# Kernel tuning notes

Measured on AMD Instinct MI355X. Metric: run time of the kernel, lower is better.

Reference implementation:

```python
import jax, jax.numpy as jnp
import numpy as np

N_NODES = 100000
N_EDGES = 1600000
IN_DIM = 128
HEADS = 4
CHANNELS = 32          # hidden_size // heads = 128 // 4
OUT_DIM = 32           # output_size of last GATConv
NEG_SLOPE = 0.2        # DGL GATConv default leaky_relu slope


def setup_inputs() -> dict:
    key = jax.random.key(0)
    ks = jax.random.split(key, 16)
    x = jax.random.normal(ks[0], (N_NODES, IN_DIM), dtype=jnp.float32)
    src = jax.random.randint(ks[1], (N_EDGES,), 0, N_NODES, dtype=jnp.int32)
    dst = jax.random.randint(ks[2], (N_EDGES,), 0, N_NODES, dtype=jnp.int32)

    def glorot(k, shape):
        fan = shape[0] + shape[-1]
        return jax.random.normal(k, shape, dtype=jnp.float32) * np.sqrt(2.0 / fan)

    # layer 0: in=128 -> 4 heads x 32
    W1 = glorot(ks[3], (IN_DIM, HEADS * CHANNELS))
    al1 = glorot(ks[4], (HEADS, CHANNELS))
    ar1 = glorot(ks[5], (HEADS, CHANNELS))
    W2 = glorot(ks[6], (HEADS * CHANNELS, HEADS * CHANNELS))
    al2 = glorot(ks[7], (HEADS, CHANNELS))
    ar2 = glorot(ks[8], (HEADS, CHANNELS))
    W3 = glorot(ks[9], (HEADS * CHANNELS, HEADS * OUT_DIM))
    al3 = glorot(ks[10], (HEADS, OUT_DIM))
    ar3 = glorot(ks[11], (HEADS, OUT_DIM))
    # final FC: (output_size*heads=128) -> 8
    Wfc = glorot(ks[12], (HEADS * OUT_DIM, 8))
    bfc = jnp.zeros((8,), dtype=jnp.float32)
    return {"x": x, "src": src, "dst": dst,
            "W1": W1, "al1": al1, "ar1": ar1,
            "W2": W2, "al2": al2, "ar2": ar2,
            "W3": W3, "al3": al3, "ar3": ar3,
            "Wfc": Wfc, "bfc": bfc}


def gat_layer(x, W, a_l, a_r, src, dst, activation):
    """DGL-style GATConv: fused gather / attend / segment-softmax / scatter-add."""
    n = x.shape[0]
    h, c = a_l.shape
    feat = (x @ W).reshape(n, h, c)                       # [N,H,C]
    el = jnp.einsum("nhc,hc->nh", feat, a_l)               # [N,H]
    er = jnp.einsum("nhc,hc->nh", feat, a_r)               # [N,H]
    e = jax.nn.leaky_relu(el[src] + er[dst], NEG_SLOPE)    # [E,H] per-edge logits
    # segment softmax over incoming edges of each dst node
    emax = jax.ops.segment_max(e, dst, num_segments=n)     # [N,H]
    ee = jnp.exp(e - emax[dst])                            # [E,H]
    denom = jax.ops.segment_sum(ee, dst, num_segments=n)   # [N,H]
    alpha = ee / denom[dst]                                # [E,H]
    msg = feat[src] * alpha[:, :, None]                    # [E,H,C]
    out = jax.ops.segment_sum(msg, dst, num_segments=n)    # [N,H,C]
    if activation is not None:
        out = activation(out)
    return out.reshape(n, h * c)


def reference(x, src, dst, W1, al1, ar1, W2, al2, ar2, W3, al3, ar3, Wfc, bfc):
    src = src.astype(jnp.int32)
    dst = dst.astype(jnp.int32)
    h = gat_layer(x, W1, al1, ar1, src, dst, jax.nn.relu)
    h = gat_layer(h, W2, al2, ar2, src, dst, jax.nn.relu)
    h = gat_layer(h, W3, al3, ar3, src, dst, None)         # [N, OUT_DIM*HEADS]
    h = jax.nn.relu(h)                                     # dropout p=0 -> identity
    pooled = jnp.max(h, axis=0, keepdims=True)             # graph max-pool readout [1, 128]
    logits = pooled @ Wfc + bfc                            # [1, 8]
    return jax.nn.softmax(logits, axis=-1)
```

## Files before the change

### kernel.cpp

```cpp
#include <hip/hip_runtime.h>

#define NN 100000
#define NE 1600000
#define FD 128
#define NB 391
#define CAP 4800
#define CHUNK 8192
#define GB 782
#define NPB 16
#define FBLK 6250
#define PBLK2 128

typedef __attribute__((ext_vector_type(8))) short bf16x8;
typedef __attribute__((ext_vector_type(4))) float f32x4;

union B8 { bf16x8 v; unsigned int u[4]; };


__device__ __forceinline__ unsigned short f2bf(float x) {
    unsigned int u = __float_as_uint(x);
    u += 0x7fffu + ((u >> 16) & 1u);
    return (unsigned short)(u >> 16);
}

__device__ __forceinline__ unsigned char f2fp8(float x) {
    return (unsigned char)__builtin_amdgcn_cvt_pk_fp8_f32(x, 0.f, 0u, false);
}

__device__ __forceinline__ unsigned int pkhi(unsigned int ua, unsigned int ub) {
    return __builtin_amdgcn_perm(ub, ua, 0x07060302);
}

__device__ __forceinline__ void split8(const float4& x0, const float4& x1,
                                       bf16x8& hi, bf16x8& lo) {
    float f[8] = {x0.x, x0.y, x0.z, x0.w, x1.x, x1.y, x1.z, x1.w};
    B8 H, L;
#pragma unroll
    for (int i = 0; i < 4; i++) {
        unsigned int ua = __float_as_uint(f[2 * i]);
        unsigned int ub = __float_as_uint(f[2 * i + 1]);
        H.u[i] = pkhi(ua, ub);
        float ra = f[2 * i]     - __uint_as_float(ua & 0xffff0000u);
        float rb = f[2 * i + 1] - __uint_as_float(ub & 0xffff0000u);
        L.u[i] = pkhi(__float_as_uint(ra), __float_as_uint(rb));
    }
    hi = H.v; lo = L.v;
}


__global__ void k_wsplit3(const float* __restrict__ W1, const float* __restrict__ W2,
                          const float* __restrict__ W3, unsigned short* __restrict__ Wth,
                          unsigned short* __restrict__ Wtl, int* __restrict__ gcur) {
    int gid = blockIdx.x * 256 + threadIdx.x;
    if (gid < NB) gcur[gid] = 0;
    int w = gid >> 14;
    int tid = gid & 16383;
    const float* W = (w == 0) ? W1 : (w == 1) ? W2 : W3;
    int n = tid >> 7, k = tid & 127;
    float val = W[k * 128 + n];
    unsigned short h = f2bf(val);
    float res = val - __uint_as_float((unsigned int)h << 16);
    Wth[gid] = h;
    Wtl[gid] = f2bf(res);
}


__global__ __launch_bounds__(256) void k_bucket(const int* __restrict__ src,
                                                const int* __restrict__ dst,
                                                int* __restrict__ gcur,
                                                unsigned int* __restrict__ pairs) {
    __shared__ int scnt[NB];
    __shared__ int sbase[NB];
    int t = threadIdx.x;
    for (int i = t; i < NB; i += 256) scnt[i] = 0;
    __syncthreads();
    int e0 = blockIdx.x * CHUNK, e1 = min(e0 + CHUNK, NE);
    for (int i = e0 + t; i < e1; i += 256) atomicAdd(&scnt[dst[i] >> 8], 1);
    __syncthreads();
    for (int i = t; i < NB; i += 256) {
        int c = scnt[i];
        sbase[i] = (c > 0) ? (i * CAP + atomicAdd(&gcur[i], c)) : 0;
        scnt[i] = 0;
    }
    __syncthreads();
    for (int i = e0 + t; i < e1; i += 256) {
        int d = dst[i];
        int b = d >> 8;
        int r = atomicAdd(&scnt[b], 1);
        pairs[sbase[b] + r] = (unsigned int)src[i] | ((unsigned int)(d & 255) << 17);
    }
}


__device__ void bsort_body(int b, const unsigned int* __restrict__ pairs,
                           const int* __restrict__ gcur, int* __restrict__ off,
                           int* __restrict__ deg, int* __restrict__ ssrc) {
    __shared__ int hcnt[256];
    __shared__ int cur[256];
    int t = threadIdx.x;
    int cnt = gcur[b];
    int estart = b * CAP;
    hcnt[t] = 0;
    __syncthreads();
    for (int i = t; i < cnt; i += 256)
        atomicAdd(&hcnt[(pairs[estart + i] >> 17) & 255], 1);
    __syncthreads();
    int v = hcnt[t];
    cur[t] = v;
    __syncthreads();
    for (int o = 1; o < 256; o <<= 1) {
        int x = (t >= o) ? cur[t - o] : 0;
        __syncthreads();
        cur[t] += x;
        __syncthreads();
    }
    int excl = cur[t] - v;
    int node = (b << 8) + t;
    if (node < NN) {
        off[node] = estart + excl;
        deg[node] = v;
    }
    __syncthreads();
    cur[t] = estart + excl;
    __syncthreads();
    for (int i = t; i < cnt; i += 256) {
        unsigned int p = pairs[estart + i];
        int pos = atomicAdd(&cur[(p >> 17) & 255], 1);
        ssrc[pos] = (int)(p & 0x1ffffu);
    }
}


__device__ __forceinline__ void epilogue(f32x4 acc[2][8], int row0, int q, int r, int nrows,
                                         const float* __restrict__ al,
                                         const float* __restrict__ ar,
                                         unsigned char* __restrict__ FbG,
                                         float* __restrict__ el, float* __restrict__ er,
                                         unsigned char* __restrict__ sg8, int lane) {
#pragma unroll
    for (int g = 0; g < 2; g++) {
#pragma unroll
        for (int i = 0; i < 4; i++) {
            int row_l = g * 16 + q * 4 + i;
            int row = row0 + row_l;
            float elp[4], erp[4];
#pragma unroll
            for (int h = 0; h < 4; h++) { elp[h] = 0.f; erp[h] = 0.f; }
#pragma unroll
            for (int nt = 0; nt < 8; nt++) {
                int h = nt >> 1;
                int c = ((nt & 1) << 4) + r;
                float v = acc[g][nt][i];
                elp[h] = fmaf(v, al[h * 32 + c], elp[h]);
                erp[h] = fmaf(v, ar[h * 32 + c], erp[h]);
            }
#pragma unroll
            for (int o = 1; o < 16; o <<= 1) {
#pragma unroll
                for (int h = 0; h < 4; h++) {
                    elp[h] += __shfl_xor(elp[h], o);
                    erp[h] += __shfl_xor(erp[h], o);
                }
            }
#pragma unroll
            for (int nt = 0; nt < 8; nt++)
                sg8[row_l * 128 + nt * 16 + r] = f2fp8(acc[g][nt][i]);
            if (row < nrows) {
                int hh = r & 3;
                float ve = (hh & 2) ? ((hh & 1) ? elp[3] : elp[2]) : ((hh & 1) ? elp[1] : elp[0]);
                float vr = (hh & 2) ? ((hh & 1) ? erp[3] : erp[2]) : ((hh & 1) ? erp[1] : erp[0]);
                if (r < 4) el[row * 4 + hh] = ve;
                else if (r < 8) er[row * 4 + hh] = vr;
            }
        }
    }
#pragma unroll
    for (int it = 0; it < 4; it++) {
        int off = it * 1024 + lane * 16;
        int row = row0 + (off >> 7);
        uint4 v = *(const uint4*)(sg8 + off);
        if (row < nrows) *(uint4*)(FbG + (size_t)row * FD + (off & 127)) = v;
    }
}


__device__ void gemm_f32_body(int bid, const float* __restrict__ A,
                              const unsigned short* __restrict__ Wth,
                              const unsigned short* __restrict__ Wtl,
                              unsigned char* __restrict__ Fb, int nrows,
                              const float* __restrict__ al, const float* __restrict__ ar,
                              float* __restrict__ el, float* __restrict__ er) {
    __shared__ unsigned char sg8[4][4096];
    int t = threadIdx.x;
    int wave = t >> 6, lane = t & 63;
    int r = lane & 15, q = lane >> 4;
    int row0 = bid * 128 + wave * 32;
    int rg0 = row0 + r, rg1 = row0 + 16 + r;

    f32x4 acc[2][8];
#pragma unroll
    for (int g = 0; g < 2; g++)
#pragma unroll
        for (int nt = 0; nt < 8; nt++) acc[g][nt] = (f32x4){0.f, 0.f, 0.f, 0.f};

#pragma unroll
    for (int ks = 0; ks < 4; ks++) {
        int k0 = ks * 32 + q * 8;
        float4 z = make_float4(0.f, 0.f, 0.f, 0.f);
        float4 a0 = z, a1 = z, b0 = z, b1 = z;
        if (rg0 < nrows) {
            const float* pa = A + (size_t)rg0 * FD + k0;
            a0 = *(const float4*)pa;
            a1 = *(const float4*)(pa + 4);
        }
        if (rg1 < nrows) {
            const float* pb = A + (size_t)rg1 * FD + k0;
            b0 = *(const float4*)pb;
            b1 = *(const float4*)(pb + 4);
        }
        bf16x8 ah0, al0, ah1, al1;
        split8(a0, a1, ah0, al0);
        split8(b0, b1, ah1, al1);
#pragma unroll
        for (int nt = 0; nt < 8; nt++) {
            int wo = ((nt * 16 + r) << 7) + k0;
            bf16x8 bh = *(const bf16x8*)(Wth + wo);
            bf16x8 bl = *(const bf16x8*)(Wtl + wo);
            acc[0][nt] = __builtin_amdgcn_mfma_f32_16x16x32_bf16(ah0, bh, acc[0][nt], 0, 0, 0);
            acc[0][nt] = __builtin_amdgcn_mfma_f32_16x16x32_bf16(al0, bh, acc[0][nt], 0, 0, 0);
            acc[0][nt] = __builtin_amdgcn_mfma_f32_16x16x32_bf16(ah0, bl, acc[0][nt], 0, 0, 0);
            acc[1][nt] = __builtin_amdgcn_mfma_f32_16x16x32_bf16(ah1, bh, acc[1][nt], 0, 0, 0);
            acc[1][nt] = __builtin_amdgcn_mfma_f32_16x16x32_bf16(al1, bh, acc[1][nt], 0, 0, 0);
            acc[1][nt] = __builtin_amdgcn_mfma_f32_16x16x32_bf16(ah1, bl, acc[1][nt], 0, 0, 0);
        }
    }
    epilogue(acc, row0, q, r, nrows, al, ar, Fb, el, er, sg8[wave], lane);
}


__global__ __launch_bounds__(256) void k_sortgemm1(const unsigned int* __restrict__ pairs,
                                                   const int* __restrict__ gcur,
                                                   int* __restrict__ off, int* __restrict__ deg,
                                                   int* __restrict__ ssrc,
                                                   const float* __restrict__ A,
                                                   const unsigned short* __restrict__ Wth,
                                                   const unsigned short* __restrict__ Wtl,
                                                   unsigned char* __restrict__ Fb,
                                                   const float* __restrict__ al,
                                                   const float* __restrict__ ar,
                                                   float* __restrict__ el,
                                                   float* __restrict__ er) {
    int b = blockIdx.x;
    if (b < NB) bsort_body(b, pairs, gcur, off, deg, ssrc);
    else gemm_f32_body(b - NB, A, Wth, Wtl, Fb, NN, al, ar, el, er);
}


__device__ __forceinline__ void agg_node(int d,
        const unsigned char* __restrict__ Fb,
        const float* __restrict__ el, const float* __restrict__ er,
        const int* __restrict__ off, const int* __restrict__ deg_,
        const int* __restrict__ ssrc, int lane, float acc8[8]) {
#pragma unroll
    for (int z = 0; z < 8; z++) acc8[z] = 0.f;
    int start = off[d];
    int dg = deg_[d];
    if (dg > 0) {
        int h = lane & 3;
        int eloc = lane >> 2;
        int g = lane >> 4;
        int c16 = lane & 15;
        int hsel2 = c16 >> 2;
        float er_h = er[d * 4 + h];
        float s = 0.f;
        for (int base = 0; base < dg; base += 16) {
            int i = base + eloc;
            float a = 0.f;
            int sid = 0;
            if (i < dg) {
                sid = ssrc[start + i];
                float v = el[sid * 4 + h] + er_h;
                float e = v > 0.f ? v : 0.2f * v;
                a = __expf(e);
            }
            s += a;
#pragma unroll
            for (int k = 0; k < 4; k++) {
                int sl = 16 * k + 4 * g;
                int sid_v = __shfl(sid, sl, 64);
                float av = __shfl(a, sl + hsel2, 64);
                uint2 u = *(const uint2*)(Fb + (size_t)sid_v * FD + c16 * 8);
                {
                    auto p = __builtin_amdgcn_cvt_pk_f32_fp8(u.x, false);
                    acc8[0] = fmaf(av, p[0], acc8[0]);
                    acc8[1] = fmaf(av, p[1], acc8[1]);
                }
                {
                    auto p = __builtin_amdgcn_cvt_pk_f32_fp8(u.x, true);
                    acc8[2] = fmaf(av, p[0], acc8[2]);
                    acc8[3] = fmaf(av, p[1], acc8[3]);
                }
                {
                    auto p = __builtin_amdgcn_cvt_pk_f32_fp8(u.y, false);
                    acc8[4] = fmaf(av, p[0], acc8[4]);
                    acc8[5] = fmaf(av, p[1], acc8[5]);
                }
                {
                    auto p = __builtin_amdgcn_cvt_pk_f32_fp8(u.y, true);
                    acc8[6] = fmaf(av, p[0], acc8[6]);
                    acc8[7] = fmaf(av, p[1], acc8[7]);
                }
            }
        }
#pragma unroll
        for (int z = 0; z < 8; z++) {
            acc8[z] += __shfl_xor(acc8[z], 16, 64);
            acc8[z] += __shfl_xor(acc8[z], 32, 64);
        }
        for (int o = 4; o < 64; o <<= 1) s += __shfl_xor(s, o, 64);
        float inv = 1.f / __shfl(s, hsel2, 64);
#pragma unroll
        for (int z = 0; z < 8; z++) acc8[z] *= inv;
    }
#pragma unroll
    for (int z = 0; z < 8; z++) acc8[z] = fmaxf(acc8[z], 0.f);
}


__global__ __launch_bounds__(1024, 8) void k_agggemm2(
        const unsigned char* __restrict__ Fb,
        const float* __restrict__ el, const float* __restrict__ er,
        const int* __restrict__ off, const int* __restrict__ deg_,
        const int* __restrict__ ssrc,
        const unsigned short* __restrict__ Wth,
        const unsigned short* __restrict__ Wtl,
        unsigned char* __restrict__ Fbn,
        const float* __restrict__ aln, const float* __restrict__ arn,
        float* __restrict__ eln, float* __restrict__ ern) {
    __shared__ unsigned char lds[NPB * 256];
    __shared__ unsigned char lds8[NPB * 128];
    int t = threadIdx.x;
    int w = t >> 6, lane = t & 63;
    int c16 = lane & 15, g = lane >> 4;
    int row0 = blockIdx.x * NPB;
    int d = row0 + w;

    float acc8[8];
    if (d < NN) {
        agg_node(d, Fb, el, er, off, deg_, ssrc, lane, acc8);
    } else {
#pragma unroll
        for (int z = 0; z < 8; z++) acc8[z] = 0.f;
    }
    if (g == 0) {
        uint4 pk;
        pk.x = ((unsigned int)f2bf(acc8[1]) << 16) | f2bf(acc8[0]);
        pk.y = ((unsigned int)f2bf(acc8[3]) << 16) | f2bf(acc8[2]);
        pk.z = ((unsigned int)f2bf(acc8[5]) << 16) | f2bf(acc8[4]);
        pk.w = ((unsigned int)f2bf(acc8[7]) << 16) | f2bf(acc8[6]);
        int boff = (w * 256 + c16 * 16) ^ ((w & 7) << 4);
        *(uint4*)(lds + boff) = pk;
    }
    __syncthreads();

    if (w < 4) {
        int r = c16, q = g;
        f32x4 acc[2];
        acc[0] = (f32x4){0.f, 0.f, 0.f, 0.f};
        acc[1] = (f32x4){0.f, 0.f, 0.f, 0.f};
#pragma unroll
        for (int ks = 0; ks < 4; ks++) {
            int aoff = (r * 256 + ks * 64 + q * 16) ^ ((r & 7) << 4);
            bf16x8 a = *(const bf16x8*)(lds + aoff);
            int k0 = ks * 32 + q * 8;
#pragma unroll
            for (int nl = 0; nl < 2; nl++) {
                int nt = 2 * w + nl;
                int wo = ((nt * 16 + r) << 7) + k0;
                bf16x8 bh = *(const bf16x8*)(Wth + wo);
                bf16x8 bl = *(const bf16x8*)(Wtl + wo);
                acc[nl] = __builtin_amdgcn_mfma_f32_16x16x32_bf16(a, bh, acc[nl], 0, 0, 0);
                acc[nl] = __builtin_amdgcn_mfma_f32_16x16x32_bf16(a, bl, acc[nl], 0, 0, 0);
            }
        }
#pragma unroll
        for (int i = 0; i < 4; i++) {
            int row_l = q * 4 + i;
            int row = row0 + row_l;
            float elp = 0.f, erp = 0.f;
#pragma unroll
            for (int nl = 0; nl < 2; nl++) {
                int c = (nl << 4) + r;
                float v = acc[nl][i];
                elp = fmaf(v, aln[w * 32 + c], elp);
                erp = fmaf(v, arn[w * 32 + c], erp);
            }
#pragma unroll
            for (int o = 1; o < 16; o <<= 1) {
                elp += __shfl_xor(elp, o);
                erp += __shfl_xor(erp, o);
            }
#pragma unroll
            for (int nl = 0; nl < 2; nl++)
                lds8[row_l * 128 + (2 * w + nl) * 16 + r] = f2fp8(acc[nl][i]);
            if (row < NN && r == 0) {
                eln[row * 4 + w] = elp;
                ern[row * 4 + w] = erp;
            }
        }
    }
    __syncthreads();
    if (t < 128) {
        int row = row0 + (t >> 3);
        uint4 v = *(const uint4*)(lds8 + t * 16);
        if (row < NN) *(uint4*)(Fbn + (size_t)row * FD + (t & 7) * 16) = v;
    }
}


__global__ __launch_bounds__(1024, 8) void k_aggpool2(
        const unsigned char* __restrict__ Fb,
        const float* __restrict__ el, const float* __restrict__ er,
        const int* __restrict__ off, const int* __restrict__ deg_,
        const int* __restrict__ ssrc,
        float* __restrict__ partials) {
    __shared__ float wmax[NPB][128];
    int t = threadIdx.x;
    int w = t >> 6, lane = t & 63;
    int c16 = lane & 15, g = lane >> 4;
    int d = blockIdx.x * NPB + w;
    float acc8[8];
    if (d < NN) {
        agg_node(d, Fb, el, er, off, deg_, ssrc, lane, acc8);
    } else {
#pragma unroll
        for (int z = 0; z < 8; z++) acc8[z] = 0.f;
    }
    if (g == 0) {
#pragma unroll
        for (int z = 0; z < 8; z++) wmax[w][c16 * 8 + z] = acc8[z];
    }
    __syncthreads();
    if (t < 128) {
        float m = 0.f;
#pragma unroll
        for (int i = 0; i < NPB; i++) m = fmaxf(m, wmax[i][t]);
        partials[(size_t)blockIdx.x * 128 + t] = m;
    }
}


__global__ __launch_bounds__(128) void k_poolred(const float* __restrict__ partials,
                                                 float* __restrict__ partials2) {
    int c = threadIdx.x;
    int b = blockIdx.x;
    float m = 0.f;
    for (int r = b; r < FBLK; r += PBLK2)
        m = fmaxf(m, partials[(size_t)r * 128 + c]);
    partials2[(size_t)b * 128 + c] = m;
}


__global__ __launch_bounds__(1024) void k_final(const float* __restrict__ partials2,
                                                const float* __restrict__ Wfc,
                                                const float* __restrict__ bfc,
                                                float* __restrict__ outp) {
    __shared__ float red[1024];
    int t = threadIdx.x;
    int c = t & 127;
    int slice = t >> 7;
    float m = 0.f;
    int i0 = slice * (PBLK2 / 8);
#pragma unroll
    for (int k = 0; k < PBLK2 / 8; ++k)
        m = fmaxf(m, partials2[(size_t)(i0 + k) * 128 + c]);
    red[t] = m;
    __syncthreads();
    if (t < 128) {
        float v = red[t];
#pragma unroll
        for (int s = 1; s < 8; ++s) v = fmaxf(v, red[s * 128 + t]);
        red[t] = __uint_as_float((unsigned int)f2bf(v) << 16);
    }
    __syncthreads();
    if (t < 64) {
        int j = t & 7;
        int kk = t >> 3;
        float partial = 0.f;
        for (int k = kk * 16; k < kk * 16 + 16; ++k) partial += red[k] * Wfc[k * 8 + j];
        for (int o = 8; o < 64; o <<= 1) partial += __shfl_xor(partial, o);
        float logit = partial + bfc[j];
        float mxl = logit;
        for (int o = 1; o < 8; o <<= 1) mxl = fmaxf(mxl, __shfl_xor(mxl, o));
        float ex = __expf(logit - mxl);
        float sm = ex;
        for (int o = 1; o < 8; o <<= 1) sm += __shfl_xor(sm, o);
        if (t < 8) outp[t] = ex / sm;
    }
}


extern "C" void kernel_launch(void* const* d_in, const int* in_sizes, int n_in,
                              void* d_out, int out_size, void* d_ws, size_t ws_size,
                              hipStream_t stream) {
    const float* x   = (const float*)d_in[0];
    const int*   src = (const int*)d_in[1];
    const int*   dst = (const int*)d_in[2];
    const float* W1  = (const float*)d_in[3];
    const float* al1 = (const float*)d_in[4];
    const float* ar1 = (const float*)d_in[5];
    const float* W2  = (const float*)d_in[6];
    const float* al2 = (const float*)d_in[7];
    const float* ar2 = (const float*)d_in[8];
    const float* W3  = (const float*)d_in[9];
    const float* al3 = (const float*)d_in[10];
    const float* ar3 = (const float*)d_in[11];
    const float* Wfc = (const float*)d_in[12];
    const float* bfc = (const float*)d_in[13];
    float* out = (float*)d_out;

    char* p = (char*)d_ws;
    auto alloc = [&](size_t bytes) {
        char* r = p;
        p += (bytes + 255) & ~(size_t)255;
        return r;
    };
    unsigned char* Fb_a = (unsigned char*)alloc((size_t)NN * FD);
    unsigned char* Fb_b = (unsigned char*)alloc((size_t)NN * FD);
    float* el_a   = (float*)alloc((size_t)NN * 4 * 4);
    float* er_a   = (float*)alloc((size_t)NN * 4 * 4);
    int*   off    = (int*)alloc((size_t)NN * 4);
    int*   deg    = (int*)alloc((size_t)NN * 4);
    int*   ssrc   = (int*)alloc((size_t)NB * CAP * 4);
    unsigned int* pairs = (unsigned int*)alloc((size_t)NB * CAP * 4);
    int*   gcur   = (int*)alloc((size_t)NB * 4);
    float* partials  = (float*)alloc((size_t)FBLK * 128 * 4);
    float* partials2 = (float*)alloc((size_t)PBLK2 * 128 * 4);
    unsigned short* Wth = (unsigned short*)alloc(3 * 16384 * 2);
    unsigned short* Wtl = (unsigned short*)alloc(3 * 16384 * 2);
    float* el_b = (float*)pairs;
    float* er_b = (float*)pairs + (size_t)NN * 4;

    const int BB = (NE + CHUNK - 1) / CHUNK;

    k_wsplit3<<<192, 256, 0, stream>>>(W1, W2, W3, Wth, Wtl, gcur);
    k_bucket<<<BB, 256, 0, stream>>>(src, dst, gcur, pairs);

    k_sortgemm1<<<NB + GB, 256, 0, stream>>>(pairs, gcur, off, deg, ssrc,
                                             x, Wth, Wtl, Fb_a, al1, ar1, el_a, er_a);
    k_agggemm2<<<FBLK, 1024, 0, stream>>>(Fb_a, el_a, er_a, off, deg, ssrc,
                                          Wth + 16384, Wtl + 16384, Fb_b, al2, ar2, el_b, er_b);
    k_agggemm2<<<FBLK, 1024, 0, stream>>>(Fb_b, el_b, er_b, off, deg, ssrc,
                                          Wth + 32768, Wtl + 32768, Fb_a, al3, ar3, el_a, er_a);
    k_aggpool2<<<FBLK, 1024, 0, stream>>>(Fb_a, el_a, er_a, off, deg, ssrc, partials);
    k_poolred<<<PBLK2, 128, 0, stream>>>(partials, partials2);
    k_final<<<1, 1024, 0, stream>>>(partials2, Wfc, bfc, out);
}
```

Before: 504.5 us.

## Split fused aggregate+GEMM into separate aggregation and GEMM kernels with small blocks

```diff
diff --git a/kernel.cpp b/kernel.cpp
--- a/kernel.cpp
+++ b/kernel.cpp
@@ -7,9 +7,8 @@
 #define CAP 4800
 #define CHUNK 8192
 #define GB 782
-#define NPB 16
-#define FBLK 6250
-#define PBLK2 128
+#define AB 25000
+#define PBLK2 512
 
 typedef __attribute__((ext_vector_type(8))) short bf16x8;
 typedef __attribute__((ext_vector_type(4))) float f32x4;
@@ -327,108 +326,83 @@
 }
 
 
-__global__ __launch_bounds__(1024, 8) void k_agggemm2(
+__global__ __launch_bounds__(256) void k_agg8(
         const unsigned char* __restrict__ Fb,
         const float* __restrict__ el, const float* __restrict__ er,
         const int* __restrict__ off, const int* __restrict__ deg_,
         const int* __restrict__ ssrc,
-        const unsigned short* __restrict__ Wth,
-        const unsigned short* __restrict__ Wtl,
-        unsigned char* __restrict__ Fbn,
-        const float* __restrict__ aln, const float* __restrict__ arn,
-        float* __restrict__ eln, float* __restrict__ ern) {
-    __shared__ unsigned char lds[NPB * 256];
-    __shared__ unsigned char lds8[NPB * 128];
-    int t = threadIdx.x;
-    int w = t >> 6, lane = t & 63;
+        unsigned int* __restrict__ Hb) {
+    int wave = threadIdx.x >> 6, lane = threadIdx.x & 63;
+    int d = blockIdx.x * 4 + wave;
+    if (d >= NN) return;
+    float acc8[8];
+    agg_node(d, Fb, el, er, off, deg_, ssrc, lane, acc8);
     int c16 = lane & 15, g = lane >> 4;
-    int row0 = blockIdx.x * NPB;
-    int d = row0 + w;
-
-    float acc8[8];
-    if (d < NN) {
-        agg_node(d, Fb, el, er, off, deg_, ssrc, lane, acc8);
-    } else {
-#pragma unroll
-        for (int z = 0; z < 8; z++) acc8[z] = 0.f;
-    }
     if (g == 0) {
         uint4 pk;
         pk.x = ((unsigned int)f2bf(acc8[1]) << 16) | f2bf(acc8[0]);
         pk.y = ((unsigned int)f2bf(acc8[3]) << 16) | f2bf(acc8[2]);
         pk.z = ((unsigned int)f2bf(acc8[5]) << 16) | f2bf(acc8[4]);
         pk.w = ((unsigned int)f2bf(acc8[7]) << 16) | f2bf(acc8[6]);
-        int boff = (w * 256 + c16 * 16) ^ ((w & 7) << 4);
-        *(uint4*)(lds + boff) = pk;
-    }
-    __syncthreads();
-
-    if (w < 4) {
-        int r = c16, q = g;
-        f32x4 acc[2];
-        acc[0] = (f32x4){0.f, 0.f, 0.f, 0.f};
-        acc[1] = (f32x4){0.f, 0.f, 0.f, 0.f};
-#pragma unroll
-        for (int ks = 0; ks < 4; ks++) {
-            int aoff = (r * 256 + ks * 64 + q * 16) ^ ((r & 7) << 4);
-            bf16x8 a = *(const bf16x8*)(lds + aoff);
-            int k0 = ks * 32 + q * 8;
-#pragma unroll
-            for (int nl = 0; nl < 2; nl++) {
-                int nt = 2 * w + nl;
-                int wo = ((nt * 16 + r) << 7) + k0;
-                bf16x8 bh = *(const bf16x8*)(Wth + wo);
-                bf16x8 bl = *(const bf16x8*)(Wtl + wo);
-                acc[nl] = __builtin_amdgcn_mfma_f32_16x16x32_bf16(a, bh, acc[nl], 0, 0, 0);
-                acc[nl] = __builtin_amdgcn_mfma_f32_16x16x32_bf16(a, bl, acc[nl], 0, 0, 0);
-            }
-        }
-#pragma unroll
-        for (int i = 0; i < 4; i++) {
-            int row_l = q * 4 + i;
-            int row = row0 + row_l;
-            float elp = 0.f, erp = 0.f;
-#pragma unroll
-            for (int nl = 0; nl < 2; nl++) {
-                int c = (nl << 4) + r;
-                float v = acc[nl][i];
-                elp = fmaf(v, aln[w * 32 + c], elp);
-                erp = fmaf(v, arn[w * 32 + c], erp);
-            }
-#pragma unroll
-            for (int o = 1; o < 16; o <<= 1) {
-                elp += __shfl_xor(elp, o);
-                erp += __shfl_xor(erp, o);
-            }
-#pragma unroll
-            for (int nl = 0; nl < 2; nl++)
-                lds8[row_l * 128 + (2 * w + nl) * 16 + r] = f2fp8(acc[nl][i]);
-            if (row < NN && r == 0) {
-                eln[row * 4 + w] = elp;
-                ern[row * 4 + w] = erp;
-            }
-        }
-    }
-    __syncthreads();
-    if (t < 128) {
-        int row = row0 + (t >> 3);
-        uint4 v = *(const uint4*)(lds8 + t * 16);
-        if (row < NN) *(uint4*)(Fbn + (size_t)row * FD + (t & 7) * 16) = v;
-    }
-}
-
-
-__global__ __launch_bounds__(1024, 8) void k_aggpool2(
+        *(uint4*)(Hb + (size_t)d * 64 + c16 * 4) = pk;
+    }
+}
+
+
+__global__ __launch_bounds__(256) void k_gemm8(const unsigned short* __restrict__ A,
+                                               const unsigned short* __restrict__ Wth,
+                                               const unsigned short* __restrict__ Wtl,
+                                               unsigned char* __restrict__ Fb,
+                                               const float* __restrict__ al,
+                                               const float* __restrict__ ar,
+                                               float* __restrict__ el,
+                                               float* __restrict__ er) {
+    __shared__ unsigned char sg8[4][4096];
+    int t = threadIdx.x;
+    int wave = t >> 6, lane = t & 63;
+    int r = lane & 15, q = lane >> 4;
+    int row0 = blockIdx.x * 128 + wave * 32;
+    int rg0 = row0 + r, rg1 = row0 + 16 + r;
+
+    f32x4 acc[2][8];
+#pragma unroll
+    for (int g = 0; g < 2; g++)
+#pragma unroll
+        for (int nt = 0; nt < 8; nt++) acc[g][nt] = (f32x4){0.f, 0.f, 0.f, 0.f};
+
+#pragma unroll
+    for (int ks = 0; ks < 4; ks++) {
+        int k0 = ks * 32 + q * 8;
+        bf16x8 a0 = {0, 0, 0, 0, 0, 0, 0, 0};
+        bf16x8 a1 = {0, 0, 0, 0, 0, 0, 0, 0};
+        if (rg0 < NN) a0 = *(const bf16x8*)(A + (size_t)rg0 * FD + k0);
+        if (rg1 < NN) a1 = *(const bf16x8*)(A + (size_t)rg1 * FD + k0);
+#pragma unroll
+        for (int nt = 0; nt < 8; nt++) {
+            int wo = ((nt * 16 + r) << 7) + k0;
+            bf16x8 bh = *(const bf16x8*)(Wth + wo);
+            bf16x8 bl = *(const bf16x8*)(Wtl + wo);
+            acc[0][nt] = __builtin_amdgcn_mfma_f32_16x16x32_bf16(a0, bh, acc[0][nt], 0, 0, 0);
+            acc[0][nt] = __builtin_amdgcn_mfma_f32_16x16x32_bf16(a0, bl, acc[0][nt], 0, 0, 0);
+            acc[1][nt] = __builtin_amdgcn_mfma_f32_16x16x32_bf16(a1, bh, acc[1][nt], 0, 0, 0);
+            acc[1][nt] = __builtin_amdgcn_mfma_f32_16x16x32_bf16(a1, bl, acc[1][nt], 0, 0, 0);
+        }
+    }
+    epilogue(acc, row0, q, r, NN, al, ar, Fb, el, er, sg8[wave], lane);
+}
+
+
+__global__ __launch_bounds__(256) void k_aggpool8(
         const unsigned char* __restrict__ Fb,
         const float* __restrict__ el, const float* __restrict__ er,
         const int* __restrict__ off, const int* __restrict__ deg_,
         const int* __restrict__ ssrc,
         float* __restrict__ partials) {
-    __shared__ float wmax[NPB][128];
+    __shared__ float wmax[4][128];
     int t = threadIdx.x;
-    int w = t >> 6, lane = t & 63;
+    int wave = t >> 6, lane = t & 63;
     int c16 = lane & 15, g = lane >> 4;
-    int d = blockIdx.x * NPB + w;
+    int d = blockIdx.x * 4 + wave;
     float acc8[8];
     if (d < NN) {
         agg_node(d, Fb, el, er, off, deg_, ssrc, lane, acc8);
@@ -438,13 +412,11 @@
     }
     if (g == 0) {
 #pragma unroll
-        for (int z = 0; z < 8; z++) wmax[w][c16 * 8 + z] = acc8[z];
+        for (int z = 0; z < 8; z++) wmax[wave][c16 * 8 + z] = acc8[z];
     }
     __syncthreads();
     if (t < 128) {
-        float m = 0.f;
-#pragma unroll
-        for (int i = 0; i < NPB; i++) m = fmaxf(m, wmax[i][t]);
+        float m = fmaxf(fmaxf(wmax[0][t], wmax[1][t]), fmaxf(wmax[2][t], wmax[3][t]));
         partials[(size_t)blockIdx.x * 128 + t] = m;
     }
 }
@@ -454,8 +426,10 @@
                                                  float* __restrict__ partials2) {
     int c = threadIdx.x;
     int b = blockIdx.x;
+    const int R = (AB + PBLK2 - 1) / PBLK2;
+    int r0 = b * R, r1 = min(AB, r0 + R);
     float m = 0.f;
-    for (int r = b; r < FBLK; r += PBLK2)
+    for (int r = r0; r < r1; ++r)
         m = fmaxf(m, partials[(size_t)r * 128 + c]);
     partials2[(size_t)b * 128 + c] = m;
 }
@@ -527,6 +501,7 @@
     };
     unsigned char* Fb_a = (unsigned char*)alloc((size_t)NN * FD);
     unsigned char* Fb_b = (unsigned char*)alloc((size_t)NN * FD);
+    unsigned int*  Hb   = (unsigned int*)alloc((size_t)NN * 64 * 4);
     float* el_a   = (float*)alloc((size_t)NN * 4 * 4);
     float* er_a   = (float*)alloc((size_t)NN * 4 * 4);
     int*   off    = (int*)alloc((size_t)NN * 4);
@@ -534,7 +509,7 @@
     int*   ssrc   = (int*)alloc((size_t)NB * CAP * 4);
     unsigned int* pairs = (unsigned int*)alloc((size_t)NB * CAP * 4);
     int*   gcur   = (int*)alloc((size_t)NB * 4);
-    float* partials  = (float*)alloc((size_t)FBLK * 128 * 4);
+    float* partials  = (float*)alloc((size_t)AB * 128 * 4);
     float* partials2 = (float*)alloc((size_t)PBLK2 * 128 * 4);
     unsigned short* Wth = (unsigned short*)alloc(3 * 16384 * 2);
     unsigned short* Wtl = (unsigned short*)alloc(3 * 16384 * 2);
@@ -548,11 +523,13 @@
 
     k_sortgemm1<<<NB + GB, 256, 0, stream>>>(pairs, gcur, off, deg, ssrc,
                                              x, Wth, Wtl, Fb_a, al1, ar1, el_a, er_a);
-    k_agggemm2<<<FBLK, 1024, 0, stream>>>(Fb_a, el_a, er_a, off, deg, ssrc,
-                                          Wth + 16384, Wtl + 16384, Fb_b, al2, ar2, el_b, er_b);
-    k_agggemm2<<<FBLK, 1024, 0, stream>>>(Fb_b, el_b, er_b, off, deg, ssrc,
-                                          Wth + 32768, Wtl + 32768, Fb_a, al3, ar3, el_a, er_a);
-    k_aggpool2<<<FBLK, 1024, 0, stream>>>(Fb_a, el_a, er_a, off, deg, ssrc, partials);
+    k_agg8<<<AB, 256, 0, stream>>>(Fb_a, el_a, er_a, off, deg, ssrc, Hb);
+    k_gemm8<<<GB, 256, 0, stream>>>((const unsigned short*)Hb, Wth + 16384, Wtl + 16384,
+                                    Fb_b, al2, ar2, el_b, er_b);
+    k_agg8<<<AB, 256, 0, stream>>>(Fb_b, el_b, er_b, off, deg, ssrc, Hb);
+    k_gemm8<<<GB, 256, 0, stream>>>((const unsigned short*)Hb, Wth + 32768, Wtl + 32768,
+                                    Fb_a, al3, ar3, el_a, er_a);
+    k_aggpool8<<<AB, 256, 0, stream>>>(Fb_a, el_a, er_a, off, deg, ssrc, partials);
     k_poolred<<<PBLK2, 128, 0, stream>>>(partials, partials2);
     k_final<<<1, 1024, 0, stream>>>(partials2, Wfc, bfc, out);
 }
```

Result: faster. 475.6 us (-5.7%).
